# Kernel optimization log

Measured on AMD Instinct MI355X. Metric: run time of the kernel, lower is better.

The kernel has to match this reference:

```python
import jax, jax.numpy as jnp
import numpy as np

N = 50000
E = 640000
NFEAT = 128
NHID = 128
ALPHA = 0.2  # leaky relu slope


def setup_inputs() -> dict:
    key = jax.random.key(0)
    k1, k2, k3, k4, k5 = jax.random.split(key, 5)
    x = jax.random.normal(k1, (N, NFEAT), dtype=jnp.float32)
    W = jax.random.normal(k2, (NFEAT, NHID), dtype=jnp.float32) * (1.0 / np.sqrt(NFEAT))
    a = jax.random.normal(k3, (1, 2 * NHID), dtype=jnp.float32) * 0.1
    # every node appears at least once as a source so rowsum > 0 (as in a real adjacency)
    src = jnp.concatenate([jnp.arange(N, dtype=jnp.int64 if jax.config.read('jax_enable_x64') else jnp.int32),
                           jax.random.randint(k4, (E - N,), 0, N)]).astype(jnp.int32)
    dst = jax.random.randint(k5, (E,), 0, N).astype(jnp.int32)
    edge_index = jnp.stack([src, dst], axis=0)
    return {"x": x, "W": W, "a": a, "edge_index": edge_index, "no_need_param": 0}


def reference(x, W, a, edge_index, no_need_param):
    # SpGraphAttentionLayer (concat=False), single head
    h = x @ W                                   # [N, nhid]
    src, dst = edge_index[0], edge_index[1]     # [E]
    nhid = W.shape[1]
    a1, a2 = a[0, :nhid], a[0, nhid:]
    # a @ cat(h[src], h[dst])  ==  h[src]@a1 + h[dst]@a2
    score = h[src] @ a1 + h[dst] @ a2           # [E]
    e = jnp.exp(-jax.nn.leaky_relu(score, ALPHA))
    n = x.shape[0]
    rowsum = jax.ops.segment_sum(e, src, num_segments=n)              # [N]
    h_prime = jax.ops.segment_sum(e[:, None] * h[dst], src, num_segments=n)  # [N, nhid]
    neighborhood_emb = h_prime / (rowsum[:, None] + 1e-16)
    # fused combine: elu(x @ W - neighborhood aggregation)
    mapped_fea = x @ W
    return jax.nn.elu(mapped_fea - neighborhood_emb)
```

## Files before the change

kernel.cpp:

```cpp
#include <hip/hip_runtime.h>
#include <hip/hip_fp16.h>
#include <math.h>

#define NFEAT 128
#define NHID  128
#define ALPHA 0.2f
#define CAP   64

typedef __attribute__((ext_vector_type(8))) short short8;
typedef __attribute__((ext_vector_type(4))) float f32x4;
typedef __attribute__((ext_vector_type(4))) int   i32x4;

__device__ inline unsigned int pack_bf16x2_rn(float x, float y) {
    unsigned int bx = __float_as_uint(x), by = __float_as_uint(y);
    bx += 0x7fffu + ((bx >> 16) & 1u);
    by += 0x7fffu + ((by >> 16) & 1u);
    return (bx >> 16) | (by & 0xffff0000u);
}

union Frag { unsigned int u[4]; uint4 v; short8 s; };

__global__ __launch_bounds__(256) void prep_wt_kernel(
    const float* __restrict__ W, unsigned int* __restrict__ Wtg,
    int* __restrict__ cnt, int n)
{
    const int t = threadIdx.x;

    if (blockIdx.x >= 16) {
        const int n4     = n >> 2;
        const int stride = (gridDim.x - 16) << 8;
        int4* h4 = (int4*)cnt;
        for (int i = (blockIdx.x - 16) * 256 + t; i < n4; i += stride)
            h4[i] = make_int4(0, 0, 0, 0);
        for (int i = (n4 << 2) + (blockIdx.x - 16) * 256 + t; i < n; i += stride)
            cnt[i] = 0;
        return;
    }

    __shared__ float tile[32][33];
    const int kt = blockIdx.x >> 2;
    const int nt = blockIdx.x & 3;

    {
        const int r = t >> 3, c = t & 7;
        const float4 v = *((const float4*)&W[(size_t)(kt * 32 + r) * NHID + nt * 32 + c * 4]);
        tile[r][c * 4 + 0] = v.x; tile[r][c * 4 + 1] = v.y;
        tile[r][c * 4 + 2] = v.z; tile[r][c * 4 + 3] = v.w;
    }
    __syncthreads();

    const int nn = t & 31;
    #pragma unroll
    for (int i = 0; i < 2; ++i) {
        const int kk = (t >> 5) * 2 + i;
        Wtg[(size_t)(nt * 32 + nn) * 64 + kt * 16 + kk] =
            pack_bf16x2_rn(tile[kk * 2][nn], tile[kk * 2 + 1][nn]);
    }
}

__global__ __launch_bounds__(256) void gemm_h_kernel(
    const float* __restrict__ x, const unsigned int* __restrict__ Wtg,
    const float* __restrict__ a, unsigned int* __restrict__ hbu,
    float* __restrict__ s1, float* __restrict__ s2, int n)
{
    __shared__ unsigned int Wtu[128 * 64];

    const int t = threadIdx.x;

    #pragma unroll
    for (int i = 0; i < 8; ++i) {
        const int u  = i * 256 + t;
        const uint4 v = ((const uint4*)Wtg)[u];
        const int nn = u >> 4, kc = u & 15;
        *((uint4*)&Wtu[nn * 64 + (kc ^ (nn & 15)) * 4]) = v;
    }

    const int w    = t >> 6;
    const int lane = t & 63;
    const int c    = lane & 15;
    const int quad = lane >> 4;

    const int rowbase = blockIdx.x * 64 + w * 16;

    int arow = rowbase + c; if (arow >= n) arow = n - 1;
    const f32x4* xp = (const f32x4*)(x + (size_t)arow * NFEAT);
    f32x4 xv[8];
    #pragma unroll
    for (int s = 0; s < 4; ++s) {
        xv[2 * s]     = __builtin_nontemporal_load(&xp[s * 8 + quad * 2]);
        xv[2 * s + 1] = __builtin_nontemporal_load(&xp[s * 8 + quad * 2 + 1]);
    }

    float a1v[8], a2v[8];
    #pragma unroll
    for (int tt = 0; tt < 8; ++tt) {
        a1v[tt] = a[tt * 16 + c];
        a2v[tt] = a[NHID + tt * 16 + c];
    }

    f32x4 acc[8];
    #pragma unroll
    for (int tt = 0; tt < 8; ++tt) acc[tt] = (f32x4){0.f, 0.f, 0.f, 0.f};

    __syncthreads();

    #pragma unroll
    for (int s = 0; s < 4; ++s) {
        Frag afr;
        afr.u[0] = pack_bf16x2_rn(xv[2 * s].x,     xv[2 * s].y);
        afr.u[1] = pack_bf16x2_rn(xv[2 * s].z,     xv[2 * s].w);
        afr.u[2] = pack_bf16x2_rn(xv[2 * s + 1].x, xv[2 * s + 1].y);
        afr.u[3] = pack_bf16x2_rn(xv[2 * s + 1].z, xv[2 * s + 1].w);
        const int kc = s * 4 + quad;
        #pragma unroll
        for (int tt = 0; tt < 8; ++tt) {
            Frag bfr;
            bfr.v = *((const uint4*)&Wtu[(tt * 16 + c) * 64 + (kc ^ c) * 4]);
            acc[tt] = __builtin_amdgcn_mfma_f32_16x16x32_bf16(
                afr.s, bfr.s, acc[tt], 0, 0, 0);
        }
    }

    #pragma unroll
    for (int r = 0; r < 4; ++r) {
        const int  row = rowbase + quad * 4 + r;
        const bool ok  = (row < n);
        float p1 = 0.f, p2 = 0.f;
        #pragma unroll
        for (int tt = 0; tt < 8; ++tt) {
            const float v = acc[tt][r];
            p1 = fmaf(v, a1v[tt], p1);
            p2 = fmaf(v, a2v[tt], p2);
        }
        if (ok) {
            uint4 pk;
            pk.x = pack_bf16x2_rn(acc[0][r], acc[1][r]);
            pk.y = pack_bf16x2_rn(acc[2][r], acc[3][r]);
            pk.z = pack_bf16x2_rn(acc[4][r], acc[5][r]);
            pk.w = pack_bf16x2_rn(acc[6][r], acc[7][r]);
            *((uint4*)&hbu[(size_t)row * 64 + c * 4]) = pk;
        }
        #pragma unroll
        for (int off = 1; off <= 8; off <<= 1) {
            p1 += __shfl_xor(p1, off, 64);
            p2 += __shfl_xor(p2, off, 64);
        }
        if (ok && c == 0) { s1[row] = p1; s2[row] = p2; }
    }
}

__global__ __launch_bounds__(256) void scatter_kernel(
    const int* __restrict__ ei, const float* __restrict__ s1,
    const float* __restrict__ s2, int* __restrict__ cnt,
    unsigned int* __restrict__ erec, int E)
{
    const int E4  = E >> 2;
    const int i   = blockIdx.x * 256 + threadIdx.x;

    if (i < E4) {
        const i32x4 s4 = __builtin_nontemporal_load(&((const i32x4*)ei)[i]);
        const i32x4 d4 = __builtin_nontemporal_load(&((const i32x4*)(ei + E))[i]);
        const int sa[4] = { s4.x, s4.y, s4.z, s4.w };
        const int da[4] = { d4.x, d4.y, d4.z, d4.w };
        #pragma unroll
        for (int k = 0; k < 4; ++k) {
            float s = s1[sa[k]] + s2[da[k]];
            s = (s > 0.f) ? s : ALPHA * s;
            const float ev = expf(-s);
            const unsigned int evh = (unsigned int)__half_as_ushort(__float2half(ev));
            const int pos = atomicAdd(&cnt[sa[k]], 1);
            if (pos < CAP)
                erec[(size_t)sa[k] * CAP + pos] = ((unsigned int)da[k] << 16) | evh;
        }
    }
    const int tail = E - (E4 << 2);
    if (blockIdx.x == 0 && threadIdx.x < tail) {
        const int j = (E4 << 2) + threadIdx.x;
        const int src = ei[j];
        const int dst = ei[E + j];
        float s = s1[src] + s2[dst];
        s = (s > 0.f) ? s : ALPHA * s;
        const float ev = expf(-s);
        const unsigned int evh = (unsigned int)__half_as_ushort(__float2half(ev));
        const int pos = atomicAdd(&cnt[src], 1);
        if (pos < CAP)
            erec[(size_t)src * CAP + pos] = ((unsigned int)dst << 16) | evh;
    }
}

__global__ __launch_bounds__(256) void aggregate_kernel(
    const int* __restrict__ cnt, const unsigned int* __restrict__ erec,
    const unsigned int* __restrict__ hbu, float* __restrict__ out, int n)
{
    const int node = (blockIdx.x * 256 + threadIdx.x) >> 4;
    const int l    = threadIdx.x & 15;
    if (node >= n) return;

    const int beg = node * CAP;
    int deg = cnt[node]; if (deg > CAP) deg = CAP;
    const int end = beg + deg;

    float acc[8];
    #pragma unroll
    for (int i = 0; i < 8; ++i) acc[i] = 0.f;
    float rs = 0.f;

    const uint4* hbu4 = (const uint4*)hbu;

    #define BL(x) __uint_as_float((x) << 16)
    #define BH(x) __uint_as_float((x) & 0xffff0000u)
    #define ACC4(u, ev)                                   \
        acc[0] = fmaf(ev, BL(u.x), acc[0]);               \
        acc[4] = fmaf(ev, BH(u.x), acc[4]);               \
        acc[1] = fmaf(ev, BL(u.y), acc[1]);               \
        acc[5] = fmaf(ev, BH(u.y), acc[5]);               \
        acc[2] = fmaf(ev, BL(u.z), acc[2]);               \
        acc[6] = fmaf(ev, BH(u.z), acc[6]);               \
        acc[3] = fmaf(ev, BL(u.w), acc[3]);               \
        acc[7] = fmaf(ev, BH(u.w), acc[7]);

    int e = beg;
    for (; e + 8 <= end; e += 8) {
        unsigned int rr[8];
        uint4 u[8];
        #pragma unroll
        for (int i = 0; i < 8; ++i) rr[i] = erec[e + i];
        #pragma unroll
        for (int i = 0; i < 8; ++i)
            u[i] = hbu4[(size_t)(rr[i] >> 16) * 16 + l];
        #pragma unroll
        for (int i = 0; i < 8; ++i) {
            const float ev = __half2float(__ushort_as_half((unsigned short)(rr[i] & 0xffffu)));
            ACC4(u[i], ev);
            rs += ev;
        }
    }
    for (; e + 2 <= end; e += 2) {
        const unsigned int r0 = erec[e], r1 = erec[e + 1];
        const uint4 u0 = hbu4[(size_t)(r0 >> 16) * 16 + l];
        const uint4 u1 = hbu4[(size_t)(r1 >> 16) * 16 + l];
        const float e0 = __half2float(__ushort_as_half((unsigned short)(r0 & 0xffffu)));
        const float e1 = __half2float(__ushort_as_half((unsigned short)(r1 & 0xffffu)));
        ACC4(u0, e0); ACC4(u1, e1);
        rs += e0 + e1;
    }
    if (e < end) {
        const unsigned int r0 = erec[e];
        const uint4 u0 = hbu4[(size_t)(r0 >> 16) * 16 + l];
        const float e0 = __half2float(__ushort_as_half((unsigned short)(r0 & 0xffffu)));
        ACC4(u0, e0);
        rs += e0;
    }
    #undef ACC4

    const float rinv = 1.0f / (rs + 1e-16f);
    const uint4 us = hbu4[(size_t)node * 16 + l];
    float* op = out + (size_t)node * NHID + l;
    float z;
    z = BL(us.x) - acc[0] * rinv; __builtin_nontemporal_store((z > 0.f) ? z : (expf(z) - 1.f), op);
    z = BH(us.x) - acc[4] * rinv; __builtin_nontemporal_store((z > 0.f) ? z : (expf(z) - 1.f), op + 16);
    z = BL(us.y) - acc[1] * rinv; __builtin_nontemporal_store((z > 0.f) ? z : (expf(z) - 1.f), op + 32);
    z = BH(us.y) - acc[5] * rinv; __builtin_nontemporal_store((z > 0.f) ? z : (expf(z) - 1.f), op + 48);
    z = BL(us.z) - acc[2] * rinv; __builtin_nontemporal_store((z > 0.f) ? z : (expf(z) - 1.f), op + 64);
    z = BH(us.z) - acc[6] * rinv; __builtin_nontemporal_store((z > 0.f) ? z : (expf(z) - 1.f), op + 80);
    z = BL(us.w) - acc[3] * rinv; __builtin_nontemporal_store((z > 0.f) ? z : (expf(z) - 1.f), op + 96);
    z = BH(us.w) - acc[7] * rinv; __builtin_nontemporal_store((z > 0.f) ? z : (expf(z) - 1.f), op + 112);
    #undef BL
    #undef BH
}

extern "C" void kernel_launch(void* const* d_in, const int* in_sizes, int n_in,
                              void* d_out, int out_size, void* d_ws, size_t ws_size,
                              hipStream_t stream) {
    const float* x  = (const float*)d_in[0];
    const float* W  = (const float*)d_in[1];
    const float* a  = (const float*)d_in[2];
    const int*   ei = (const int*)d_in[3];

    const int n = in_sizes[0] / NFEAT;
    const int E = in_sizes[3] / 2;

    float* out = (float*)d_out;

    unsigned int* hbu  = (unsigned int*)d_ws;
    float*        s1   = (float*)(hbu + (size_t)n * 64);
    float*        s2   = s1 + n;
    unsigned int* erec = (unsigned int*)(s2 + n);
    unsigned int* Wtg  = erec + (size_t)n * CAP;
    int*          cnt  = (int*)(Wtg + 8192);

    prep_wt_kernel<<<16 + 50, 256, 0, stream>>>(W, Wtg, cnt, n);

    const int gemm_blocks = (n + 63) / 64;
    gemm_h_kernel<<<gemm_blocks, 256, 0, stream>>>(x, Wtg, a, hbu, s1, s2, n);

    const int E4 = E >> 2;
    scatter_kernel<<<(E4 + 255) / 256, 256, 0, stream>>>(ei, s1, s2, cnt, erec, E);

    aggregate_kernel<<<((size_t)n * 16 + 255) / 256, 256, 0, stream>>>(
        cnt, erec, hbu, out, n);
}
```

Baseline: 153.8 us.

## Fuse edge scatter into GEMM launch and compute attention weights in aggregate

Edge bucketing by source no longer needs the attention scores, so it now runs as extra blocks inside the GEMM launch, overlapping with the projection and removing one kernel launch. Each edge record shrinks to a 16-bit destination index. The leaky-relu/exp weight is recomputed in the aggregate kernel from s1 and a gathered s2. This removes one launch, a serial dependency and half the edge-record traffic. In exchange it adds an s2 gather and expf that all 16 lanes of a node repeat for every edge, and it relies on node ids fitting in 16 bits.

Measured after the change: 154.2 us. Within noise of the previous version (+0.3%).

```diff
diff --git a/kernel.cpp b/kernel.cpp
--- a/kernel.cpp
+++ b/kernel.cpp
@@ -58,14 +58,43 @@
     }
 }
 
-__global__ __launch_bounds__(256) void gemm_h_kernel(
+__global__ __launch_bounds__(256) void gemm_scatter_kernel(
     const float* __restrict__ x, const unsigned int* __restrict__ Wtg,
     const float* __restrict__ a, unsigned int* __restrict__ hbu,
-    float* __restrict__ s1, float* __restrict__ s2, int n)
+    float* __restrict__ s1, float* __restrict__ s2, int n,
+    const int* __restrict__ ei, int* __restrict__ cnt,
+    unsigned short* __restrict__ erec, int E, int scat_blocks)
 {
     __shared__ unsigned int Wtu[128 * 64];
 
     const int t = threadIdx.x;
+
+    if ((int)blockIdx.x < scat_blocks) {
+        const int E4 = E >> 2;
+        const int i  = blockIdx.x * 256 + t;
+        if (i < E4) {
+            const i32x4 s4 = __builtin_nontemporal_load(&((const i32x4*)ei)[i]);
+            const i32x4 d4 = __builtin_nontemporal_load(&((const i32x4*)(ei + E))[i]);
+            const int sa[4] = { s4.x, s4.y, s4.z, s4.w };
+            const int da[4] = { d4.x, d4.y, d4.z, d4.w };
+            #pragma unroll
+            for (int k = 0; k < 4; ++k) {
+                const int pos = atomicAdd(&cnt[sa[k]], 1);
+                if (pos < CAP)
+                    erec[(size_t)sa[k] * CAP + pos] = (unsigned short)da[k];
+            }
+        }
+        const int tail = E - (E4 << 2);
+        if (blockIdx.x == 0 && t < tail) {
+            const int j   = (E4 << 2) + t;
+            const int src = ei[j];
+            const int dst = ei[E + j];
+            const int pos = atomicAdd(&cnt[src], 1);
+            if (pos < CAP)
+                erec[(size_t)src * CAP + pos] = (unsigned short)dst;
+        }
+        return;
+    }
 
     #pragma unroll
     for (int i = 0; i < 8; ++i) {
@@ -80,7 +109,7 @@
     const int c    = lane & 15;
     const int quad = lane >> 4;
 
-    const int rowbase = blockIdx.x * 64 + w * 16;
+    const int rowbase = (blockIdx.x - scat_blocks) * 64 + w * 16;
 
     int arow = rowbase + c; if (arow >= n) arow = n - 1;
     const f32x4* xp = (const f32x4*)(x + (size_t)arow * NFEAT);
@@ -149,56 +178,18 @@
     }
 }
 
-__global__ __launch_bounds__(256) void scatter_kernel(
-    const int* __restrict__ ei, const float* __restrict__ s1,
-    const float* __restrict__ s2, int* __restrict__ cnt,
-    unsigned int* __restrict__ erec, int E)
-{
-    const int E4  = E >> 2;
-    const int i   = blockIdx.x * 256 + threadIdx.x;
-
-    if (i < E4) {
-        const i32x4 s4 = __builtin_nontemporal_load(&((const i32x4*)ei)[i]);
-        const i32x4 d4 = __builtin_nontemporal_load(&((const i32x4*)(ei + E))[i]);
-        const int sa[4] = { s4.x, s4.y, s4.z, s4.w };
-        const int da[4] = { d4.x, d4.y, d4.z, d4.w };
-        #pragma unroll
-        for (int k = 0; k < 4; ++k) {
-            float s = s1[sa[k]] + s2[da[k]];
-            s = (s > 0.f) ? s : ALPHA * s;
-            const float ev = expf(-s);
-            const unsigned int evh = (unsigned int)__half_as_ushort(__float2half(ev));
-            const int pos = atomicAdd(&cnt[sa[k]], 1);
-            if (pos < CAP)
-                erec[(size_t)sa[k] * CAP + pos] = ((unsigned int)da[k] << 16) | evh;
-        }
-    }
-    const int tail = E - (E4 << 2);
-    if (blockIdx.x == 0 && threadIdx.x < tail) {
-        const int j = (E4 << 2) + threadIdx.x;
-        const int src = ei[j];
-        const int dst = ei[E + j];
-        float s = s1[src] + s2[dst];
-        s = (s > 0.f) ? s : ALPHA * s;
-        const float ev = expf(-s);
-        const unsigned int evh = (unsigned int)__half_as_ushort(__float2half(ev));
-        const int pos = atomicAdd(&cnt[src], 1);
-        if (pos < CAP)
-            erec[(size_t)src * CAP + pos] = ((unsigned int)dst << 16) | evh;
-    }
-}
-
 __global__ __launch_bounds__(256) void aggregate_kernel(
-    const int* __restrict__ cnt, const unsigned int* __restrict__ erec,
-    const unsigned int* __restrict__ hbu, float* __restrict__ out, int n)
+    const int* __restrict__ cnt, const unsigned short* __restrict__ erec,
+    const unsigned int* __restrict__ hbu, const float* __restrict__ s1,
+    const float* __restrict__ s2, float* __restrict__ out, int n)
 {
     const int node = (blockIdx.x * 256 + threadIdx.x) >> 4;
     const int l    = threadIdx.x & 15;
     if (node >= n) return;
 
-    const int beg = node * CAP;
     int deg = cnt[node]; if (deg > CAP) deg = CAP;
-    const int end = beg + deg;
+    const unsigned short* rp = erec + (size_t)node * CAP;
+    const float s1n = s1[node];
 
     float acc[8];
     #pragma unroll
@@ -218,40 +209,55 @@
         acc[6] = fmaf(ev, BH(u.z), acc[6]);               \
         acc[3] = fmaf(ev, BL(u.w), acc[3]);               \
         acc[7] = fmaf(ev, BH(u.w), acc[7]);
-
-    int e = beg;
-    for (; e + 8 <= end; e += 8) {
-        unsigned int rr[8];
+    #define EV(d_, ev_)                                   \
+        float sc_ = s1n + s2[d_];                         \
+        sc_ = (sc_ > 0.f) ? sc_ : ALPHA * sc_;            \
+        const float ev_ = expf(-sc_);
+
+    int e = 0;
+    for (; e + 8 <= deg; e += 8) {
+        const uint4 rv = *((const uint4*)(rp + e));
+        int d[8];
+        d[0] = rv.x & 0xffffu; d[1] = rv.x >> 16;
+        d[2] = rv.y & 0xffffu; d[3] = rv.y >> 16;
+        d[4] = rv.z & 0xffffu; d[5] = rv.z >> 16;
+        d[6] = rv.w & 0xffffu; d[7] = rv.w >> 16;
+        float sv[8];
+        #pragma unroll
+        for (int i = 0; i < 8; ++i) sv[i] = s2[d[i]];
         uint4 u[8];
         #pragma unroll
-        for (int i = 0; i < 8; ++i) rr[i] = erec[e + i];
-        #pragma unroll
-        for (int i = 0; i < 8; ++i)
-            u[i] = hbu4[(size_t)(rr[i] >> 16) * 16 + l];
+        for (int i = 0; i < 8; ++i) u[i] = hbu4[(size_t)d[i] * 16 + l];
         #pragma unroll
         for (int i = 0; i < 8; ++i) {
-            const float ev = __half2float(__ushort_as_half((unsigned short)(rr[i] & 0xffffu)));
+            float sc = s1n + sv[i];
+            sc = (sc > 0.f) ? sc : ALPHA * sc;
+            const float ev = expf(-sc);
             ACC4(u[i], ev);
             rs += ev;
         }
     }
-    for (; e + 2 <= end; e += 2) {
-        const unsigned int r0 = erec[e], r1 = erec[e + 1];
-        const uint4 u0 = hbu4[(size_t)(r0 >> 16) * 16 + l];
-        const uint4 u1 = hbu4[(size_t)(r1 >> 16) * 16 + l];
-        const float e0 = __half2float(__ushort_as_half((unsigned short)(r0 & 0xffffu)));
-        const float e1 = __half2float(__ushort_as_half((unsigned short)(r1 & 0xffffu)));
+    for (; e + 2 <= deg; e += 2) {
+        const int d0 = rp[e], d1 = rp[e + 1];
+        const float sv0 = s2[d0], sv1 = s2[d1];
+        const uint4 u0 = hbu4[(size_t)d0 * 16 + l];
+        const uint4 u1 = hbu4[(size_t)d1 * 16 + l];
+        float sc0 = s1n + sv0; sc0 = (sc0 > 0.f) ? sc0 : ALPHA * sc0;
+        float sc1 = s1n + sv1; sc1 = (sc1 > 0.f) ? sc1 : ALPHA * sc1;
+        const float e0 = expf(-sc0), e1 = expf(-sc1);
         ACC4(u0, e0); ACC4(u1, e1);
         rs += e0 + e1;
     }
-    if (e < end) {
-        const unsigned int r0 = erec[e];
-        const uint4 u0 = hbu4[(size_t)(r0 >> 16) * 16 + l];
-        const float e0 = __half2float(__ushort_as_half((unsigned short)(r0 & 0xffffu)));
+    if (e < deg) {
+        const int d0 = rp[e];
+        const uint4 u0 = hbu4[(size_t)d0 * 16 + l];
+        float sc0 = s1n + s2[d0]; sc0 = (sc0 > 0.f) ? sc0 : ALPHA * sc0;
+        const float e0 = expf(-sc0);
         ACC4(u0, e0);
         rs += e0;
     }
     #undef ACC4
+    #undef EV
 
     const float rinv = 1.0f / (rs + 1e-16f);
     const uint4 us = hbu4[(size_t)node * 16 + l];
@@ -282,21 +288,21 @@
 
     float* out = (float*)d_out;
 
-    unsigned int* hbu  = (unsigned int*)d_ws;
-    float*        s1   = (float*)(hbu + (size_t)n * 64);
-    float*        s2   = s1 + n;
-    unsigned int* erec = (unsigned int*)(s2 + n);
-    unsigned int* Wtg  = erec + (size_t)n * CAP;
-    int*          cnt  = (int*)(Wtg + 8192);
+    unsigned int*   hbu  = (unsigned int*)d_ws;
+    float*          s1   = (float*)(hbu + (size_t)n * 64);
+    float*          s2   = s1 + n;
+    unsigned short* erec = (unsigned short*)(s2 + n);
+    unsigned int*   Wtg  = (unsigned int*)(erec + (size_t)n * CAP);
+    int*            cnt  = (int*)(Wtg + 8192);
 
     prep_wt_kernel<<<16 + 50, 256, 0, stream>>>(W, Wtg, cnt, n);
 
+    const int E4          = E >> 2;
+    const int scat_blocks = (E4 + 255) / 256;
     const int gemm_blocks = (n + 63) / 64;
-    gemm_h_kernel<<<gemm_blocks, 256, 0, stream>>>(x, Wtg, a, hbu, s1, s2, n);
-
-    const int E4 = E >> 2;
-    scatter_kernel<<<(E4 + 255) / 256, 256, 0, stream>>>(ei, s1, s2, cnt, erec, E);
+    gemm_scatter_kernel<<<scat_blocks + gemm_blocks, 256, 0, stream>>>(
+        x, Wtg, a, hbu, s1, s2, n, ei, cnt, erec, E, scat_blocks);
 
     aggregate_kernel<<<((size_t)n * 16 + 255) / 256, 256, 0, stream>>>(
-        cnt, erec, hbu, out, n);
-}
+        cnt, erec, hbu, s1, s2, out, n);
+}
```

## Grid-stride scatter with batched atomics; retune nontemporal hints in gemm and aggregate

Applied to the files above, without the earlier changes.

The scatter kernel becomes a fixed 320-block grid-stride loop. Each thread handles 8 edges and issues all score gathers and all atomics before doing any dependent work, so more memory operations are in flight at once. The gemm drops nontemporal hints on its x loads, while aggregate adds nontemporal loads for the gathered neighbor rows of h. The hint changes could hurt cache reuse of h rows, which many edges share, and the fixed grid may underfill the device.

New measurement: 169.8 us. +10.4%, slower.

```diff
diff --git a/kernel.cpp b/kernel.cpp
--- a/kernel.cpp
+++ b/kernel.cpp
@@ -10,6 +10,7 @@
 typedef __attribute__((ext_vector_type(8))) short short8;
 typedef __attribute__((ext_vector_type(4))) float f32x4;
 typedef __attribute__((ext_vector_type(4))) int   i32x4;
+typedef __attribute__((ext_vector_type(4))) unsigned int u32x4;
 
 __device__ inline unsigned int pack_bf16x2_rn(float x, float y) {
     unsigned int bx = __float_as_uint(x), by = __float_as_uint(y);
@@ -87,8 +88,8 @@
     f32x4 xv[8];
     #pragma unroll
     for (int s = 0; s < 4; ++s) {
-        xv[2 * s]     = __builtin_nontemporal_load(&xp[s * 8 + quad * 2]);
-        xv[2 * s + 1] = __builtin_nontemporal_load(&xp[s * 8 + quad * 2 + 1]);
+        xv[2 * s]     = xp[s * 8 + quad * 2];
+        xv[2 * s + 1] = xp[s * 8 + quad * 2 + 1];
     }
 
     float a1v[8], a2v[8];
@@ -149,42 +150,55 @@
     }
 }
 
+#define SCAT_BLOCKS 320
+
 __global__ __launch_bounds__(256) void scatter_kernel(
     const int* __restrict__ ei, const float* __restrict__ s1,
     const float* __restrict__ s2, int* __restrict__ cnt,
     unsigned int* __restrict__ erec, int E)
 {
-    const int E4  = E >> 2;
-    const int i   = blockIdx.x * 256 + threadIdx.x;
-
-    if (i < E4) {
-        const i32x4 s4 = __builtin_nontemporal_load(&((const i32x4*)ei)[i]);
-        const i32x4 d4 = __builtin_nontemporal_load(&((const i32x4*)(ei + E))[i]);
-        const int sa[4] = { s4.x, s4.y, s4.z, s4.w };
-        const int da[4] = { d4.x, d4.y, d4.z, d4.w };
-        #pragma unroll
-        for (int k = 0; k < 4; ++k) {
-            float s = s1[sa[k]] + s2[da[k]];
-            s = (s > 0.f) ? s : ALPHA * s;
-            const float ev = expf(-s);
+    const int t      = threadIdx.x;
+    const int n8     = E >> 3;
+    const int gtid   = blockIdx.x * 256 + t;
+    const int stride = SCAT_BLOCKS << 8;
+
+    for (int i8 = gtid; i8 < n8; i8 += stride) {
+        const int e0 = i8 * 8;
+        const i32x4 sa = __builtin_nontemporal_load((const i32x4*)(ei + e0));
+        const i32x4 sb = __builtin_nontemporal_load((const i32x4*)(ei + e0 + 4));
+        const i32x4 da = __builtin_nontemporal_load((const i32x4*)(ei + E + e0));
+        const i32x4 db = __builtin_nontemporal_load((const i32x4*)(ei + E + e0 + 4));
+        const int s[8] = { sa.x, sa.y, sa.z, sa.w, sb.x, sb.y, sb.z, sb.w };
+        const int d[8] = { da.x, da.y, da.z, da.w, db.x, db.y, db.z, db.w };
+        float sv[8];
+        #pragma unroll
+        for (int k = 0; k < 8; ++k) sv[k] = s1[s[k]] + s2[d[k]];
+        int pos[8];
+        #pragma unroll
+        for (int k = 0; k < 8; ++k) pos[k] = atomicAdd(&cnt[s[k]], 1);
+        #pragma unroll
+        for (int k = 0; k < 8; ++k) {
+            float sc = sv[k];
+            sc = (sc > 0.f) ? sc : ALPHA * sc;
+            const float ev = expf(-sc);
             const unsigned int evh = (unsigned int)__half_as_ushort(__float2half(ev));
-            const int pos = atomicAdd(&cnt[sa[k]], 1);
+            if (pos[k] < CAP)
+                erec[(size_t)s[k] * CAP + pos[k]] = ((unsigned int)d[k] << 16) | evh;
+        }
+    }
+    const int tail0 = n8 << 3;
+    if (blockIdx.x == 0) {
+        for (int j = tail0 + t; j < E; j += 256) {
+            const int src = ei[j];
+            const int dst = ei[E + j];
+            float sc = s1[src] + s2[dst];
+            sc = (sc > 0.f) ? sc : ALPHA * sc;
+            const float ev = expf(-sc);
+            const unsigned int evh = (unsigned int)__half_as_ushort(__float2half(ev));
+            const int pos = atomicAdd(&cnt[src], 1);
             if (pos < CAP)
-                erec[(size_t)sa[k] * CAP + pos] = ((unsigned int)da[k] << 16) | evh;
-        }
-    }
-    const int tail = E - (E4 << 2);
-    if (blockIdx.x == 0 && threadIdx.x < tail) {
-        const int j = (E4 << 2) + threadIdx.x;
-        const int src = ei[j];
-        const int dst = ei[E + j];
-        float s = s1[src] + s2[dst];
-        s = (s > 0.f) ? s : ALPHA * s;
-        const float ev = expf(-s);
-        const unsigned int evh = (unsigned int)__half_as_ushort(__float2half(ev));
-        const int pos = atomicAdd(&cnt[src], 1);
-        if (pos < CAP)
-            erec[(size_t)src * CAP + pos] = ((unsigned int)dst << 16) | evh;
+                erec[(size_t)src * CAP + pos] = ((unsigned int)dst << 16) | evh;
+        }
     }
 }
 
@@ -205,7 +219,7 @@
     for (int i = 0; i < 8; ++i) acc[i] = 0.f;
     float rs = 0.f;
 
-    const uint4* hbu4 = (const uint4*)hbu;
+    const u32x4* hbu4 = (const u32x4*)hbu;
 
     #define BL(x) __uint_as_float((x) << 16)
     #define BH(x) __uint_as_float((x) & 0xffff0000u)
@@ -222,12 +236,12 @@
     int e = beg;
     for (; e + 8 <= end; e += 8) {
         unsigned int rr[8];
-        uint4 u[8];
+        u32x4 u[8];
         #pragma unroll
         for (int i = 0; i < 8; ++i) rr[i] = erec[e + i];
         #pragma unroll
         for (int i = 0; i < 8; ++i)
-            u[i] = hbu4[(size_t)(rr[i] >> 16) * 16 + l];
+            u[i] = __builtin_nontemporal_load(&hbu4[(size_t)(rr[i] >> 16) * 16 + l]);
         #pragma unroll
         for (int i = 0; i < 8; ++i) {
             const float ev = __half2float(__ushort_as_half((unsigned short)(rr[i] & 0xffffu)));
@@ -237,8 +251,8 @@
     }
     for (; e + 2 <= end; e += 2) {
         const unsigned int r0 = erec[e], r1 = erec[e + 1];
-        const uint4 u0 = hbu4[(size_t)(r0 >> 16) * 16 + l];
-        const uint4 u1 = hbu4[(size_t)(r1 >> 16) * 16 + l];
+        const u32x4 u0 = __builtin_nontemporal_load(&hbu4[(size_t)(r0 >> 16) * 16 + l]);
+        const u32x4 u1 = __builtin_nontemporal_load(&hbu4[(size_t)(r1 >> 16) * 16 + l]);
         const float e0 = __half2float(__ushort_as_half((unsigned short)(r0 & 0xffffu)));
         const float e1 = __half2float(__ushort_as_half((unsigned short)(r1 & 0xffffu)));
         ACC4(u0, e0); ACC4(u1, e1);
@@ -246,7 +260,7 @@
     }
     if (e < end) {
         const unsigned int r0 = erec[e];
-        const uint4 u0 = hbu4[(size_t)(r0 >> 16) * 16 + l];
+        const u32x4 u0 = __builtin_nontemporal_load(&hbu4[(size_t)(r0 >> 16) * 16 + l]);
         const float e0 = __half2float(__ushort_as_half((unsigned short)(r0 & 0xffffu)));
         ACC4(u0, e0);
         rs += e0;
@@ -254,7 +268,7 @@
     #undef ACC4
 
     const float rinv = 1.0f / (rs + 1e-16f);
-    const uint4 us = hbu4[(size_t)node * 16 + l];
+    const u32x4 us = hbu4[(size_t)node * 16 + l];
     float* op = out + (size_t)node * NHID + l;
     float z;
     z = BL(us.x) - acc[0] * rinv; __builtin_nontemporal_store((z > 0.f) ? z : (expf(z) - 1.f), op);
@@ -294,8 +308,7 @@
     const int gemm_blocks = (n + 63) / 64;
     gemm_h_kernel<<<gemm_blocks, 256, 0, stream>>>(x, Wtg, a, hbu, s1, s2, n);
 
-    const int E4 = E >> 2;
-    scatter_kernel<<<(E4 + 255) / 256, 256, 0, stream>>>(ei, s1, s2, cnt, erec, E);
+    scatter_kernel<<<SCAT_BLOCKS, 256, 0, stream>>>(ei, s1, s2, cnt, erec, E);
 
     aggregate_kernel<<<((size_t)n * 16 + 255) / 256, 256, 0, stream>>>(
         cnt, erec, hbu, out, n);
```
